# Optimization experiments

Measured on AMD Instinct MI355X. Metric: run time of the kernel, lower is better.

## Reference

```python
import jax, jax.numpy as jnp
import numpy as np

B, T, C = 4, 2048, 1024
H = 16
D = C // H  # head_size = 64


def setup_inputs() -> dict:
    key = jax.random.key(0)
    k1, k2 = jax.random.split(key)
    x = jax.random.normal(k1, (B, T, C), dtype=jnp.float32)
    w_attn = jax.random.normal(k2, (C, 3 * C), dtype=jnp.float32) * (C ** -0.5)
    return {"x": x, "w_attn": w_attn}


def reference(x, w_attn):
    Bx, Tx, Cx = x.shape
    qkv = x @ w_attn                      # [B,T,3C] (no bias)
    q, k, v = jnp.split(qkv, 3, axis=-1)  # each [B,T,C]
    # [B,T,C] -> [B,H,T,D]
    q = q.reshape(Bx, Tx, H, D).transpose(0, 2, 1, 3)
    k = k.reshape(Bx, Tx, H, D).transpose(0, 2, 1, 3)
    v = v.reshape(Bx, Tx, H, D).transpose(0, 2, 1, 3)
    wei = jnp.einsum('bhqd,bhkd->bhqk', q, k) * (D ** -0.5)  # [B,H,T,T]
    causal = jnp.tril(jnp.ones((Tx, Tx), dtype=bool))
    wei = jnp.where(causal, wei, -jnp.inf)
    wei = jax.nn.softmax(wei, axis=-1)
    out = jnp.einsum('bhqk,bhkd->bhqd', wei, v)  # [B,H,T,D]
    out = out.transpose(0, 2, 1, 3).reshape(Bx, Tx, Cx)
    return out
```

## Files before the change

kernel.cpp:

```cpp
#include <hip/hip_runtime.h>
#include <hip/hip_bf16.h>

typedef __attribute__((ext_vector_type(8))) short bf16x8;
typedef __attribute__((ext_vector_type(4))) float f32x4;

#define T_SZ 2048
#define C_SZ 1024
#define H_SZ 16
#define D_SZ 64
#define N_SZ 3072
#define M_SZ 8192

#define Q_SCALE 0.18033688011112042f

__device__ __forceinline__ unsigned short f2bf(float f) {
    unsigned int u = __float_as_uint(f);
    unsigned int r = (u + 0x7fffu + ((u >> 16) & 1u)) >> 16;
    return (unsigned short)r;
}

__device__ __forceinline__ void gload_lds16(const void* g, void* l) {
    __builtin_amdgcn_global_load_lds(
        (const __attribute__((address_space(1))) unsigned int*)g,
        (__attribute__((address_space(3))) unsigned int*)l, 16, 0, 0);
}

__global__ __launch_bounds__(256) void k_convert(const float* __restrict__ in,
                                                 unsigned short* __restrict__ out, int n4) {
    int i = blockIdx.x * 256 + threadIdx.x;
    if (i >= n4) return;
    float4 v = ((const float4*)in)[i];
    ushort4 u;
    u.x = f2bf(v.x); u.y = f2bf(v.y); u.z = f2bf(v.z); u.w = f2bf(v.w);
    ((ushort4*)out)[i] = u;
}

__global__ __launch_bounds__(256) void k_transpose(const float* __restrict__ w,
                                                   unsigned short* __restrict__ wt) {
    __shared__ float tile[32][33];
    const int nb = blockIdx.x * 32;
    const int kb = blockIdx.y * 32;
    const int tx = threadIdx.x & 31;
    const int ty = threadIdx.x >> 5;
#pragma unroll
    for (int i = 0; i < 32; i += 8)
        tile[ty + i][tx] = w[(size_t)(kb + ty + i) * N_SZ + nb + tx];
    __syncthreads();
#pragma unroll
    for (int i = 0; i < 32; i += 8)
        wt[(size_t)(nb + ty + i) * C_SZ + kb + tx] = f2bf(tile[tx][ty + i]);
}

__global__ __launch_bounds__(256) void k_qkv_gemm(const unsigned short* __restrict__ A,
                                                  const unsigned short* __restrict__ Bt,
                                                  unsigned short* __restrict__ Qb,
                                                  unsigned short* __restrict__ Kb,
                                                  unsigned short* __restrict__ Vtb) {
    __shared__ __align__(16) unsigned short As[128 * 32];
    __shared__ __align__(16) unsigned short Bs[128 * 32];
    const int id = blockIdx.x;
    const int gx = id & 7, jj = id >> 3;
    const int yblk = jj % 24;
    const int xblk = gx + 8 * (jj / 24);
    const int tid = threadIdx.x;
    const int lane = tid & 63, wid = tid >> 6;
    const int wm = wid & 1, wn = wid >> 1;
    const int row0 = xblk * 128;
    const int col0 = yblk * 128;
    f32x4 acc[4][4] = {};
    const int c0 = 2 * wid, c1 = 2 * wid + 1;
    const int lr = lane >> 2, lk = (lane & 3) * 8;
    const int l15 = lane & 15, lg = lane >> 4;

    for (int kt = 0; kt < 1024; kt += 32) {
        __syncthreads();
        gload_lds16(A + (size_t)(row0 + c0 * 16 + lr) * 1024 + kt + lk, As + c0 * 512);
        gload_lds16(A + (size_t)(row0 + c1 * 16 + lr) * 1024 + kt + lk, As + c1 * 512);
        gload_lds16(Bt + (size_t)(col0 + c0 * 16 + lr) * 1024 + kt + lk, Bs + c0 * 512);
        gload_lds16(Bt + (size_t)(col0 + c1 * 16 + lr) * 1024 + kt + lk, Bs + c1 * 512);
        __syncthreads();
        bf16x8 af[4], bfr[4];
#pragma unroll
        for (int m = 0; m < 4; ++m)
            af[m] = *(const bf16x8*)&As[(wm * 64 + m * 16 + l15) * 32 + lg * 8];
#pragma unroll
        for (int n = 0; n < 4; ++n)
            bfr[n] = *(const bf16x8*)&Bs[(wn * 64 + n * 16 + l15) * 32 + lg * 8];
#pragma unroll
        for (int m = 0; m < 4; ++m)
#pragma unroll
            for (int n = 0; n < 4; ++n)
                acc[m][n] = __builtin_amdgcn_mfma_f32_16x16x32_bf16(af[m], bfr[n], acc[m][n], 0, 0, 0);
    }

    const int sel = col0 >> 10;
    if (sel < 2) {
        unsigned short* dst = (sel == 0) ? Qb : Kb;
        const float qs = (sel == 0) ? Q_SCALE : 1.0f;
#pragma unroll
        for (int m = 0; m < 4; ++m) {
#pragma unroll
            for (int n = 0; n < 4; ++n) {
                int cc = (col0 + wn * 64 + n * 16 + l15) & 1023;
                int h = cc >> 6, d = cc & 63;
#pragma unroll
                for (int i = 0; i < 4; ++i) {
                    int row = row0 + wm * 64 + m * 16 + lg * 4 + i;
                    int b = row >> 11, t = row & 2047;
                    size_t idx = ((size_t)(b * 16 + h) * 2048 + t) * 64 + d;
                    dst[idx] = f2bf(acc[m][n][i] * qs);
                }
            }
        }
    } else {
#pragma unroll
        for (int m = 0; m < 4; ++m) {
#pragma unroll
            for (int n = 0; n < 4; ++n) {
                int cc = (col0 + wn * 64 + n * 16 + l15) & 1023;
                int h = cc >> 6, d = cc & 63;
                int row = row0 + wm * 64 + m * 16 + lg * 4;
                int b = row >> 11, t = row & 2047;
                ushort4 u;
                u.x = f2bf(acc[m][n][0]); u.y = f2bf(acc[m][n][1]);
                u.z = f2bf(acc[m][n][2]); u.w = f2bf(acc[m][n][3]);
                size_t idx = ((size_t)(b * 16 + h) * 64 + d) * 2048 + t;
                *(ushort4*)&Vtb[idx] = u;
            }
        }
    }
}

__device__ __forceinline__ void load_k(const unsigned short* __restrict__ Kp, int k0,
                                       int l15, int lg, bf16x8 kf[4][2]) {
#pragma unroll
    for (int ct = 0; ct < 4; ++ct)
#pragma unroll
        for (int kh = 0; kh < 2; ++kh)
            kf[ct][kh] = *(const bf16x8*)&Kp[(size_t)(k0 + ct * 16 + l15) * 64 + kh * 32 + lg * 8];
}

__global__ __launch_bounds__(256, 4) void k_attn(const unsigned short* __restrict__ Qb,
                                                 const unsigned short* __restrict__ Kb,
                                                 const unsigned short* __restrict__ Vt,
                                                 float* __restrict__ out) {
    const int id = blockIdx.x;
    const int g = id & 7, j = id >> 3;
    const int qb = 31 - (j & 31);
    const int bh = g + ((j >> 5) << 3);
    const int bb = bh >> 4, hh = bh & 15;
    const unsigned short* Qp = Qb + (size_t)bh * T_SZ * D_SZ;
    const unsigned short* Kp = Kb + (size_t)bh * T_SZ * D_SZ;
    const unsigned short* Vp = Vt + (size_t)bh * T_SZ * D_SZ;
    const int tid = threadIdx.x, lane = tid & 63, wid = tid >> 6;
    const int l15 = lane & 15, lg = lane >> 4;
    const int rga = qb * 64 + wid * 16;

    __shared__ __align__(16) unsigned short Pl[4][16][72];

    bf16x8 qf[2];
#pragma unroll
    for (int kh = 0; kh < 2; ++kh)
        qf[kh] = *(const bf16x8*)&Qp[(size_t)(rga + l15) * 64 + kh * 32 + lg * 8];

    f32x4 oacc[4] = {};
    float mrow[4] = {-1e30f, -1e30f, -1e30f, -1e30f};
    float lrow[4] = {0.f, 0.f, 0.f, 0.f};

    bf16x8 kf[4][2];
    load_k(Kp, 0, l15, lg, kf);

    for (int kb = 0; kb <= qb; ++kb) {
        const int k0 = kb * 64;
        bf16x8 vf[4][2];
#pragma unroll
        for (int ct = 0; ct < 4; ++ct)
#pragma unroll
            for (int kh = 0; kh < 2; ++kh)
                vf[ct][kh] = *(const bf16x8*)&Vp[(size_t)(ct * 16 + l15) * 2048 + k0 + kh * 32 + lg * 8];

        const bool act = (k0 <= rga + 15);
        f32x4 s[4];
        if (act) {
#pragma unroll
            for (int ct = 0; ct < 4; ++ct) {
                f32x4 a = {};
#pragma unroll
                for (int kh = 0; kh < 2; ++kh)
                    a = __builtin_amdgcn_mfma_f32_16x16x32_bf16(qf[kh], kf[ct][kh], a, 0, 0, 0);
                s[ct] = a;
            }
        }
        if (kb < qb) load_k(Kp, k0 + 64, l15, lg, kf);

        if (act) {
            if (k0 + 63 > rga) {
#pragma unroll
                for (int ct = 0; ct < 4; ++ct) {
                    const int key = k0 + ct * 16 + l15;
#pragma unroll
                    for (int i = 0; i < 4; ++i) {
                        const int qrow = rga + lg * 4 + i;
                        s[ct][i] = (key <= qrow) ? s[ct][i] : -1e30f;
                    }
                }
            }
#pragma unroll
            for (int i = 0; i < 4; ++i) {
                float rmax = fmaxf(fmaxf(s[0][i], s[1][i]), fmaxf(s[2][i], s[3][i]));
                rmax = fmaxf(rmax, __shfl_xor(rmax, 1));
                rmax = fmaxf(rmax, __shfl_xor(rmax, 2));
                rmax = fmaxf(rmax, __shfl_xor(rmax, 4));
                rmax = fmaxf(rmax, __shfl_xor(rmax, 8));
                float mnew = fmaxf(mrow[i], rmax);
                float sc = __builtin_amdgcn_exp2f(mrow[i] - mnew);
                float rsum = 0.f;
#pragma unroll
                for (int ct = 0; ct < 4; ++ct) {
                    float pv = __builtin_amdgcn_exp2f(s[ct][i] - mnew);
                    s[ct][i] = pv;
                    rsum += pv;
                }
                rsum += __shfl_xor(rsum, 1);
                rsum += __shfl_xor(rsum, 2);
                rsum += __shfl_xor(rsum, 4);
                rsum += __shfl_xor(rsum, 8);
                lrow[i] = lrow[i] * sc + rsum;
                mrow[i] = mnew;
#pragma unroll
                for (int ct = 0; ct < 4; ++ct) oacc[ct][i] *= sc;
            }
#pragma unroll
            for (int ct = 0; ct < 4; ++ct)
#pragma unroll
                for (int i = 0; i < 4; ++i)
                    Pl[wid][lg * 4 + i][ct * 16 + l15] = f2bf(s[ct][i]);

#pragma unroll
            for (int kh = 0; kh < 2; ++kh) {
                const bf16x8 pf = *(const bf16x8*)&Pl[wid][l15][kh * 32 + lg * 8];
#pragma unroll
                for (int ct = 0; ct < 4; ++ct)
                    oacc[ct] = __builtin_amdgcn_mfma_f32_16x16x32_bf16(pf, vf[ct][kh], oacc[ct], 0, 0, 0);
            }
        }
    }

#pragma unroll
    for (int ct = 0; ct < 4; ++ct) {
#pragma unroll
        for (int i = 0; i < 4; ++i) {
            const int qrow = rga + lg * 4 + i;
            out[((size_t)bb * T_SZ + qrow) * C_SZ + hh * 64 + ct * 16 + l15] =
                oacc[ct][i] / lrow[i];
        }
    }
}

extern "C" void kernel_launch(void* const* d_in, const int* in_sizes, int n_in,
                              void* d_out, int out_size, void* d_ws, size_t ws_size,
                              hipStream_t stream) {
    const float* x = (const float*)d_in[0];
    const float* w = (const float*)d_in[1];
    float* out = (float*)d_out;
    char* ws = (char*)d_ws;
    unsigned short* xb  = (unsigned short*)(ws);
    unsigned short* wtb = (unsigned short*)(ws + 16777216);
    unsigned short* Qb  = (unsigned short*)(ws + 16777216 + 6291456);
    unsigned short* Kb  = (unsigned short*)(ws + 16777216 + 6291456 + 16777216);
    unsigned short* Vtb = (unsigned short*)(ws + 16777216 + 6291456 + 2 * 16777216);

    k_convert<<<8192, 256, 0, stream>>>(x, xb, 2097152);
    k_transpose<<<dim3(96, 32), 256, 0, stream>>>(w, wtb);
    k_qkv_gemm<<<1536, 256, 0, stream>>>(xb, wtb, Qb, Kb, Vtb);
    k_attn<<<2048, 256, 0, stream>>>(Qb, Kb, Vtb, out);
}
```

Baseline: 429.6 us.

## Compute transposed S tile so softmax reductions stay mostly within-lane

Swaps MFMA operand order so each lane holds one query row's scores across keys. Row max and sum then need only two cross-lane shuffles instead of four per row, with per-row scale values broadcast back through shuffles. P is written to LDS as packed 64-bit stores, the diagonal mask is simplified to the last block, and the occupancy hint drops from 4 to 3 waves. It also adds a scheduling barrier after the K prefetch, which may constrain instruction interleaving.

New measurement: 408.2 us. 1.05x faster.

```diff
diff --git a/kernel.cpp b/kernel.cpp
--- a/kernel.cpp
+++ b/kernel.cpp
@@ -131,16 +131,7 @@
     }
 }
 
-__device__ __forceinline__ void load_k(const unsigned short* __restrict__ Kp, int k0,
-                                       int l15, int lg, bf16x8 kf[4][2]) {
-#pragma unroll
-    for (int ct = 0; ct < 4; ++ct)
-#pragma unroll
-        for (int kh = 0; kh < 2; ++kh)
-            kf[ct][kh] = *(const bf16x8*)&Kp[(size_t)(k0 + ct * 16 + l15) * 64 + kh * 32 + lg * 8];
-}
-
-__global__ __launch_bounds__(256, 4) void k_attn(const unsigned short* __restrict__ Qb,
+__global__ __launch_bounds__(256, 3) void k_attn(const unsigned short* __restrict__ Qb,
                                                  const unsigned short* __restrict__ Kb,
                                                  const unsigned short* __restrict__ Vt,
                                                  float* __restrict__ out) {
@@ -164,11 +155,15 @@
         qf[kh] = *(const bf16x8*)&Qp[(size_t)(rga + l15) * 64 + kh * 32 + lg * 8];
 
     f32x4 oacc[4] = {};
-    float mrow[4] = {-1e30f, -1e30f, -1e30f, -1e30f};
-    float lrow[4] = {0.f, 0.f, 0.f, 0.f};
+    float mreg = -1e30f, lreg = 0.f;
+    const int thr = wid * 16 + l15;
 
     bf16x8 kf[4][2];
-    load_k(Kp, 0, l15, lg, kf);
+#pragma unroll
+    for (int ct = 0; ct < 4; ++ct)
+#pragma unroll
+        for (int kh = 0; kh < 2; ++kh)
+            kf[ct][kh] = *(const bf16x8*)&Kp[(size_t)(ct * 16 + l15) * 64 + kh * 32 + lg * 8];
 
     for (int kb = 0; kb <= qb; ++kb) {
         const int k0 = kb * 64;
@@ -179,80 +174,90 @@
             for (int kh = 0; kh < 2; ++kh)
                 vf[ct][kh] = *(const bf16x8*)&Vp[(size_t)(ct * 16 + l15) * 2048 + k0 + kh * 32 + lg * 8];
 
-        const bool act = (k0 <= rga + 15);
-        f32x4 s[4];
-        if (act) {
-#pragma unroll
-            for (int ct = 0; ct < 4; ++ct) {
-                f32x4 a = {};
+        f32x4 st[4];
+#pragma unroll
+        for (int ct = 0; ct < 4; ++ct) {
+            f32x4 a = {};
+            a = __builtin_amdgcn_mfma_f32_16x16x32_bf16(kf[ct][0], qf[0], a, 0, 0, 0);
+            a = __builtin_amdgcn_mfma_f32_16x16x32_bf16(kf[ct][1], qf[1], a, 0, 0, 0);
+            st[ct] = a;
+        }
+        if (kb < qb) {
+#pragma unroll
+            for (int ct = 0; ct < 4; ++ct)
 #pragma unroll
                 for (int kh = 0; kh < 2; ++kh)
-                    a = __builtin_amdgcn_mfma_f32_16x16x32_bf16(qf[kh], kf[ct][kh], a, 0, 0, 0);
-                s[ct] = a;
-            }
-        }
-        if (kb < qb) load_k(Kp, k0 + 64, l15, lg, kf);
-
-        if (act) {
-            if (k0 + 63 > rga) {
-#pragma unroll
-                for (int ct = 0; ct < 4; ++ct) {
-                    const int key = k0 + ct * 16 + l15;
-#pragma unroll
-                    for (int i = 0; i < 4; ++i) {
-                        const int qrow = rga + lg * 4 + i;
-                        s[ct][i] = (key <= qrow) ? s[ct][i] : -1e30f;
-                    }
-                }
-            }
-#pragma unroll
-            for (int i = 0; i < 4; ++i) {
-                float rmax = fmaxf(fmaxf(s[0][i], s[1][i]), fmaxf(s[2][i], s[3][i]));
-                rmax = fmaxf(rmax, __shfl_xor(rmax, 1));
-                rmax = fmaxf(rmax, __shfl_xor(rmax, 2));
-                rmax = fmaxf(rmax, __shfl_xor(rmax, 4));
-                rmax = fmaxf(rmax, __shfl_xor(rmax, 8));
-                float mnew = fmaxf(mrow[i], rmax);
-                float sc = __builtin_amdgcn_exp2f(mrow[i] - mnew);
-                float rsum = 0.f;
-#pragma unroll
-                for (int ct = 0; ct < 4; ++ct) {
-                    float pv = __builtin_amdgcn_exp2f(s[ct][i] - mnew);
-                    s[ct][i] = pv;
-                    rsum += pv;
-                }
-                rsum += __shfl_xor(rsum, 1);
-                rsum += __shfl_xor(rsum, 2);
-                rsum += __shfl_xor(rsum, 4);
-                rsum += __shfl_xor(rsum, 8);
-                lrow[i] = lrow[i] * sc + rsum;
-                mrow[i] = mnew;
-#pragma unroll
-                for (int ct = 0; ct < 4; ++ct) oacc[ct][i] *= sc;
-            }
+                    kf[ct][kh] = *(const bf16x8*)&Kp[(size_t)(k0 + 64 + ct * 16 + l15) * 64 + kh * 32 + lg * 8];
+        }
+        __builtin_amdgcn_sched_barrier(0);
+
+        if (kb == qb) {
 #pragma unroll
             for (int ct = 0; ct < 4; ++ct)
 #pragma unroll
                 for (int i = 0; i < 4; ++i)
-                    Pl[wid][lg * 4 + i][ct * 16 + l15] = f2bf(s[ct][i]);
-
-#pragma unroll
-            for (int kh = 0; kh < 2; ++kh) {
-                const bf16x8 pf = *(const bf16x8*)&Pl[wid][l15][kh * 32 + lg * 8];
-#pragma unroll
-                for (int ct = 0; ct < 4; ++ct)
-                    oacc[ct] = __builtin_amdgcn_mfma_f32_16x16x32_bf16(pf, vf[ct][kh], oacc[ct], 0, 0, 0);
-            }
-        }
-    }
-
+                    if (ct * 16 + lg * 4 + i > thr) st[ct][i] = -1e30f;
+        }
+
+        float cm0 = fmaxf(fmaxf(st[0][0], st[0][1]), fmaxf(st[0][2], st[0][3]));
+        float cm1 = fmaxf(fmaxf(st[1][0], st[1][1]), fmaxf(st[1][2], st[1][3]));
+        float cm2 = fmaxf(fmaxf(st[2][0], st[2][1]), fmaxf(st[2][2], st[2][3]));
+        float cm3 = fmaxf(fmaxf(st[3][0], st[3][1]), fmaxf(st[3][2], st[3][3]));
+        float pmax = fmaxf(fmaxf(cm0, cm1), fmaxf(cm2, cm3));
+        pmax = fmaxf(pmax, __shfl_xor(pmax, 16));
+        pmax = fmaxf(pmax, __shfl_xor(pmax, 32));
+        const float mnew = fmaxf(mreg, pmax);
+        const float sc = __builtin_amdgcn_exp2f(mreg - mnew);
+        mreg = mnew;
+#pragma unroll
+        for (int ct = 0; ct < 4; ++ct)
+#pragma unroll
+            for (int i = 0; i < 4; ++i)
+                st[ct][i] = __builtin_amdgcn_exp2f(st[ct][i] - mnew);
+        float cs0 = (st[0][0] + st[0][1]) + (st[0][2] + st[0][3]);
+        float cs1 = (st[1][0] + st[1][1]) + (st[1][2] + st[1][3]);
+        float cs2 = (st[2][0] + st[2][1]) + (st[2][2] + st[2][3]);
+        float cs3 = (st[3][0] + st[3][1]) + (st[3][2] + st[3][3]);
+        float psum = (cs0 + cs1) + (cs2 + cs3);
+        psum += __shfl_xor(psum, 16);
+        psum += __shfl_xor(psum, 32);
+        lreg = lreg * sc + psum;
+
+        float scr[4];
+#pragma unroll
+        for (int i = 0; i < 4; ++i) scr[i] = __shfl(sc, lg * 4 + i, 16);
+#pragma unroll
+        for (int ct = 0; ct < 4; ++ct)
+#pragma unroll
+            for (int i = 0; i < 4; ++i) oacc[ct][i] *= scr[i];
+
+#pragma unroll
+        for (int ct = 0; ct < 4; ++ct) {
+            unsigned int lo = (unsigned int)f2bf(st[ct][0]) | ((unsigned int)f2bf(st[ct][1]) << 16);
+            unsigned int hi = (unsigned int)f2bf(st[ct][2]) | ((unsigned int)f2bf(st[ct][3]) << 16);
+            uint2 u; u.x = lo; u.y = hi;
+            *(uint2*)&Pl[wid][l15][ct * 16 + lg * 4] = u;
+        }
+
+#pragma unroll
+        for (int kh = 0; kh < 2; ++kh) {
+            const bf16x8 pf = *(const bf16x8*)&Pl[wid][l15][kh * 32 + lg * 8];
+#pragma unroll
+            for (int ct = 0; ct < 4; ++ct)
+                oacc[ct] = __builtin_amdgcn_mfma_f32_16x16x32_bf16(pf, vf[ct][kh], oacc[ct], 0, 0, 0);
+        }
+    }
+
+    float lr[4];
+#pragma unroll
+    for (int i = 0; i < 4; ++i) lr[i] = __shfl(lreg, lg * 4 + i, 16);
 #pragma unroll
     for (int ct = 0; ct < 4; ++ct) {
 #pragma unroll
         for (int i = 0; i < 4; ++i) {
             const int qrow = rga + lg * 4 + i;
             out[((size_t)bb * T_SZ + qrow) * C_SZ + hh * 64 + ct * 16 + l15] =
-                oacc[ct][i] / lrow[i];
+                oacc[ct][i] / lr[i];
         }
     }
 }
```
